# Optimization experiments

Hardware: AMD Instinct MI355X
Metric: run time of the kernel (lower is better)

## Reference

```python
import jax, jax.numpy as jnp
import numpy as np

B, S, DIN, DOUT = 4, 2048, 2048, 8192


def setup_inputs() -> dict:
    key = jax.random.key(0)
    kx, kw = jax.random.split(key)
    x = jax.random.normal(kx, (B, S, DIN), dtype=jnp.float32)
    # match torch init: uniform(-bound, bound), bound = sqrt(3) * 0.5 * in_features**-0.5
    bound = (3.0 ** 0.5) * 0.5 * DIN ** (-0.5)
    weight = jax.random.uniform(kw, (DOUT, DIN), dtype=jnp.float32, minval=-bound, maxval=bound)
    return {"x": x, "weight": weight}


def _rms_norm(x):
    # F.rms_norm with no weight: eps defaults to finfo(dtype).eps
    eps = jnp.finfo(x.dtype).eps
    return x * jax.lax.rsqrt(jnp.mean(x * x, axis=-1, keepdims=True) + eps)


def _act_quant(xn):
    # per-token int8 symmetric quant/dequant
    scale = 127.0 / jnp.maximum(jnp.max(jnp.abs(xn), axis=-1, keepdims=True), 1e-5)
    return jnp.clip(jnp.round(xn * scale), -128.0, 127.0) / scale


def _weight_quant(w):
    # ternary weight quant/dequant with global abs-mean scale
    scale = 1.0 / jnp.maximum(jnp.mean(jnp.abs(w)), 1e-5)
    return jnp.clip(jnp.round(w * scale), -1.0, 1.0) / scale


def reference(x, weight):
    xn = _rms_norm(x)
    # STE: forward uses quantized values, gradient flows through xn / weight
    x_q = xn + jax.lax.stop_gradient(_act_quant(xn) - xn)
    w_q = weight + jax.lax.stop_gradient(_weight_quant(weight) - weight)
    # F.linear: x @ w.T  -> [B, S, DOUT]
    return jnp.einsum('bsd,od->bso', x_q, w_q)
```

## Files before the change

kernel.cpp:

```cpp
#include <hip/hip_runtime.h>

typedef unsigned int u32;
typedef int i32x4 __attribute__((ext_vector_type(4)));

#define DIN 2048
#define DOUT 8192
#define MROWS 8192
#define NELEM_W (8192 * 2048)

#define WS_PART 0
#define WS_WFAC 16384
#define WS_ROWFAC 16640
#define WS_XQ 49408
#define WS_WQ (49408 + 16777216)

__global__ void k_wabs(const float* __restrict__ w, double* __restrict__ part) {
    const float4* w4 = (const float4*)w;
    const unsigned t = threadIdx.x, b = blockIdx.x;
    float s = 0.f;
    for (unsigned i = b * 256u + t; i < (NELEM_W / 4); i += 2048u * 256u) {
        float4 v = w4[i];
        s += fabsf(v.x) + fabsf(v.y) + fabsf(v.z) + fabsf(v.w);
    }
    double d = (double)s;
    #pragma unroll
    for (int o = 32; o; o >>= 1) d += __shfl_down(d, o);
    __shared__ double red[4];
    if ((t & 63u) == 0u) red[t >> 6] = d;
    __syncthreads();
    if (t == 0) part[b] = red[0] + red[1] + red[2] + red[3];
}

__global__ void k_wfin(const double* __restrict__ part, float* __restrict__ wfac) {
    const int t = threadIdx.x;
    double s = 0.0;
    #pragma unroll
    for (int j = 0; j < 8; ++j) s += part[t + j * 256];
    #pragma unroll
    for (int o = 32; o; o >>= 1) s += __shfl_down(s, o);
    __shared__ double red[4];
    if ((t & 63) == 0) red[t >> 6] = s;
    __syncthreads();
    if (t == 0) {
        double mean = (red[0] + red[1] + red[2] + red[3]) * (1.0 / (double)NELEM_W);
        *wfac = fmaxf((float)mean, 1e-5f);
    }
}

__global__ void k_prep(const float* __restrict__ w, const float* __restrict__ wfac,
                       u32* __restrict__ wq, const float* __restrict__ x,
                       u32* __restrict__ xq, float* __restrict__ rowfac) {
    const int t = threadIdx.x;
    if (blockIdx.x < 2048) {
        const float scale = 1.0f / *wfac;
        const float4* w4 = (const float4*)w;
        for (unsigned i = blockIdx.x * 256u + t; i < (NELEM_W / 4); i += 2048u * 256u) {
            float4 v = w4[i];
            int q0 = (int)fminf(fmaxf(rintf(v.x * scale), -1.f), 1.f);
            int q1 = (int)fminf(fmaxf(rintf(v.y * scale), -1.f), 1.f);
            int q2 = (int)fminf(fmaxf(rintf(v.z * scale), -1.f), 1.f);
            int q3 = (int)fminf(fmaxf(rintf(v.w * scale), -1.f), 1.f);
            wq[i] = (u32)(q0 & 255) | ((u32)(q1 & 255) << 8) |
                    ((u32)(q2 & 255) << 16) | ((u32)(q3 & 255) << 24);
        }
        return;
    }
    const int row = blockIdx.x - 2048;
    const float4* xr = (const float4*)(x + (size_t)row * DIN);
    float4 v0 = xr[t], v1 = xr[t + 256];
    float ss = v0.x * v0.x + v0.y * v0.y + v0.z * v0.z + v0.w * v0.w
             + v1.x * v1.x + v1.y * v1.y + v1.z * v1.z + v1.w * v1.w;
    __shared__ float red[4];
    #pragma unroll
    for (int o = 32; o; o >>= 1) ss += __shfl_down(ss, o);
    if ((t & 63) == 0) red[t >> 6] = ss;
    __syncthreads();
    ss = red[0] + red[1] + red[2] + red[3];
    const float r = 1.0f / sqrtf(ss * (1.0f / DIN) + 1.1920929e-7f);
    float xn[8] = {v0.x * r, v0.y * r, v0.z * r, v0.w * r,
                   v1.x * r, v1.y * r, v1.z * r, v1.w * r};
    float am = 0.f;
    #pragma unroll
    for (int j = 0; j < 8; ++j) am = fmaxf(am, fabsf(xn[j]));
    __syncthreads();
    #pragma unroll
    for (int o = 32; o; o >>= 1) am = fmaxf(am, __shfl_down(am, o));
    if ((t & 63) == 0) red[t >> 6] = am;
    __syncthreads();
    am = fmaxf(fmaxf(red[0], red[1]), fmaxf(red[2], red[3]));
    const float amc = fmaxf(am, 1e-5f);
    const float s = 127.0f / amc;
    int q[8];
    #pragma unroll
    for (int j = 0; j < 8; ++j)
        q[j] = (int)fminf(fmaxf(rintf(xn[j] * s), -128.f), 127.f);
    u32* xo = xq + (size_t)row * (DIN / 4);
    xo[t] = (u32)(q[0] & 255) | ((u32)(q[1] & 255) << 8) |
            ((u32)(q[2] & 255) << 16) | ((u32)(q[3] & 255) << 24);
    xo[t + 256] = (u32)(q[4] & 255) | ((u32)(q[5] & 255) << 8) |
                  ((u32)(q[6] & 255) << 16) | ((u32)(q[7] & 255) << 24);
    if (t == 0) rowfac[row] = amc * (1.0f / 127.0f);
}

__launch_bounds__(512, 2)
__global__ void k_gemm(const char* __restrict__ A, const char* __restrict__ Bw,
                       const float* __restrict__ rowfac, const float* __restrict__ wfac,
                       float* __restrict__ out) {
    __shared__ __attribute__((aligned(16))) char smb[131072];

    const int t = threadIdx.x;
    const int l = t & 63, w = t >> 6;
    const int wm = w >> 2, wn = w & 3;
    const int lr = l & 15, lc = l >> 4;
    const int laneRd = lr * 64 + ((lc ^ (lr & 3)) * 16);
    const int srow2 = t >> 2;
    const int sglog = ((t & 3) ^ (srow2 & 3)) * 16;

    const int bid = blockIdx.x;
    const int wg = (bid & 7) * 128 + (bid >> 3);
    const int bm = wg >> 5, bn = wg & 31;
    const char* Ab = A + (size_t)(bm * 256) * DIN;
    const char* Bb = Bw + (size_t)(bn * 256) * DIN;

    i32x4 acc[8][4] = {};
    i32x4 fa[4], fb[4];

#define STG1(gbase, opOff, tB, kh, s) do {                                        \
    _Pragma("unroll")                                                             \
    for (int j_ = 0; j_ < 2; ++j_)                                                \
        __builtin_amdgcn_global_load_lds(                                         \
            (const __attribute__((address_space(1))) void*)((gbase) + (size_t)(j_ * 128 + srow2) * DIN + (tB) + (kh) * 64 + sglog), \
            (__attribute__((address_space(3))) void*)(smb + (opOff) + (s) * 32768 + (kh) * 16384 + j_ * 8192 + t * 16), \
            16, 0, 0);                                                            \
} while (0)

#define NOGATE ((void)0)
#define VM6 asm volatile("s_waitcnt vmcnt(6)" ::: "memory")
#define VM0 asm volatile("s_waitcnt vmcnt(0)" ::: "memory")
#define NOSTG ((void)0)

#define PHASE(s, kh, mB, LOADB, STAGE_STMT, GATE_STMT) do {                       \
    const char* hbA_ = smb + (s) * 32768 + (kh) * 16384;                          \
    const char* hbB_ = hbA_ + 65536;                                              \
    _Pragma("unroll")                                                             \
    for (int i_ = 0; i_ < 4; ++i_)                                                \
        fa[i_] = *(const i32x4*)(hbA_ + (wm * 128 + ((mB) + i_) * 16) * 64 + laneRd); \
    if (LOADB) {                                                                  \
        _Pragma("unroll")                                                         \
        for (int n_ = 0; n_ < 4; ++n_)                                            \
            fb[n_] = *(const i32x4*)(hbB_ + (wn * 64 + n_ * 16) * 64 + laneRd);   \
    }                                                                             \
    STAGE_STMT;                                                                   \
    GATE_STMT;                                                                    \
    __builtin_amdgcn_s_barrier();                                                 \
    asm volatile("s_waitcnt lgkmcnt(0)" ::: "memory");                            \
    __builtin_amdgcn_s_setprio(1);                                                \
    _Pragma("unroll")                                                             \
    for (int m_ = 0; m_ < 4; ++m_)                                                \
        _Pragma("unroll")                                                         \
        for (int n_ = 0; n_ < 4; ++n_)                                            \
            acc[(mB) + m_][n_] = __builtin_amdgcn_mfma_i32_16x16x64_i8(           \
                fa[m_], fb[n_], acc[(mB) + m_][n_], 0, 0, 0);                     \
    __builtin_amdgcn_s_setprio(0);                                                \
    __builtin_amdgcn_s_barrier();                                                 \
} while (0)

    STG1(Ab, 0,     0,   0, 0);
    STG1(Bb, 65536, 0,   0, 0);
    STG1(Ab, 0,     0,   1, 0);
    STG1(Bb, 65536, 0,   1, 0);
    STG1(Bb, 65536, 128, 0, 1);
    STG1(Ab, 0,     128, 0, 1);
    STG1(Bb, 65536, 128, 1, 1);
    VM6;
    __builtin_amdgcn_s_barrier();

    #pragma unroll 1
    for (int it = 0; it < 7; ++it) {
        const int tB = it * 256;
        PHASE(0, 0, 0, true,  STG1(Ab, 0,     tB + 128, 1, 1), NOGATE);
        PHASE(0, 0, 4, false, STG1(Bb, 65536, tB + 256, 0, 0), NOGATE);
        PHASE(0, 1, 0, true,  STG1(Ab, 0,     tB + 256, 0, 0), NOGATE);
        PHASE(0, 1, 4, false, STG1(Bb, 65536, tB + 256, 1, 0), VM6);
        PHASE(1, 0, 0, true,  STG1(Ab, 0,     tB + 256, 1, 0), NOGATE);
        PHASE(1, 0, 4, false, STG1(Bb, 65536, tB + 384, 0, 1), NOGATE);
        PHASE(1, 1, 0, true,  STG1(Ab, 0,     tB + 384, 0, 1), NOGATE);
        PHASE(1, 1, 4, false, STG1(Bb, 65536, tB + 384, 1, 1), VM6);
    }
    PHASE(0, 0, 0, true,  STG1(Ab, 0, 1920, 1, 1), NOGATE);
    PHASE(0, 0, 4, false, NOSTG, NOGATE);
    PHASE(0, 1, 0, true,  NOSTG, NOGATE);
    PHASE(0, 1, 4, false, NOSTG, VM0);
    PHASE(1, 0, 0, true,  NOSTG, NOGATE);
    PHASE(1, 0, 4, false, NOSTG, NOGATE);
    PHASE(1, 1, 0, true,  NOSTG, NOGATE);
    PHASE(1, 1, 4, false, NOSTG, NOGATE);

    const float wf = *wfac;
    const int c0 = bn * 256 + wn * 64 + lr;
    #pragma unroll
    for (int m = 0; m < 8; ++m) {
        #pragma unroll
        for (int r = 0; r < 4; ++r) {
            const int grow = bm * 256 + wm * 128 + m * 16 + lc * 4 + r;
            const float s = rowfac[grow] * wf;
            const size_t ob = (size_t)grow * DOUT + c0;
            #pragma unroll
            for (int n = 0; n < 4; ++n)
                out[ob + n * 16] = (float)acc[m][n][r] * s;
        }
    }
#undef STG1
#undef PHASE
#undef NOGATE
#undef VM6
#undef VM0
#undef NOSTG
}

extern "C" void kernel_launch(void* const* d_in, const int* in_sizes, int n_in,
                              void* d_out, int out_size, void* d_ws, size_t ws_size,
                              hipStream_t stream) {
    const float* x = (const float*)d_in[0];
    const float* wt = (const float*)d_in[1];
    float* out = (float*)d_out;
    char* ws = (char*)d_ws;

    double* part = (double*)(ws + WS_PART);
    float* wfac = (float*)(ws + WS_WFAC);
    float* rowfac = (float*)(ws + WS_ROWFAC);
    u32* xq = (u32*)(ws + WS_XQ);
    u32* wq = (u32*)(ws + WS_WQ);

    k_wabs<<<2048, 256, 0, stream>>>(wt, part);
    k_wfin<<<1, 256, 0, stream>>>(part, wfac);
    k_prep<<<2048 + MROWS, 256, 0, stream>>>(wt, wfac, wq, x, xq, rowfac);
    k_gemm<<<1024, 512, 0, stream>>>((const char*)xq, (const char*)wq, rowfac, wfac, out);
}
```

Measured before the change: 216.7 us.

## Shrink GEMM tile to 128x128 with 32x32x32 int8 MFMA and 4 waves

Replaces the 256x256 block tile with 8 waves by a 128x128 tile with 4 waves, each computing a 64x64 sub-tile using 32x32x32 int8 MFMAs instead of 16x16x64. LDS use halves to 64KB, which could allow more blocks per CU, and the grid grows to 4096 blocks with a new swizzled block mapping and a reworked vmcnt-gated double-buffer schedule. The aim is better occupancy and wave balance. The cost is lower arithmetic intensity per block, meaning more global/L2 traffic for the A and B operands, plus a different epilogue store pattern.

```diff
diff --git a/kernel.cpp b/kernel.cpp
--- a/kernel.cpp
+++ b/kernel.cpp
@@ -2,6 +2,7 @@
 
 typedef unsigned int u32;
 typedef int i32x4 __attribute__((ext_vector_type(4)));
+typedef int i32x16 __attribute__((ext_vector_type(16)));
 
 #define DIN 2048
 #define DOUT 8192
@@ -102,120 +103,125 @@
     if (t == 0) rowfac[row] = amc * (1.0f / 127.0f);
 }
 
-__launch_bounds__(512, 2)
+__launch_bounds__(256, 2)
 __global__ void k_gemm(const char* __restrict__ A, const char* __restrict__ Bw,
                        const float* __restrict__ rowfac, const float* __restrict__ wfac,
                        float* __restrict__ out) {
-    __shared__ __attribute__((aligned(16))) char smb[131072];
+    __shared__ __attribute__((aligned(16))) char smb[65536];
 
     const int t = threadIdx.x;
     const int l = t & 63, w = t >> 6;
-    const int wm = w >> 2, wn = w & 3;
-    const int lr = l & 15, lc = l >> 4;
-    const int laneRd = lr * 64 + ((lc ^ (lr & 3)) * 16);
-    const int srow2 = t >> 2;
-    const int sglog = ((t & 3) ^ (srow2 & 3)) * 16;
+    const int wm = w >> 1, wn = w & 1;
+    const int la = l & 31, lhi = l >> 5;
+    const int o0 = ((lhi ^ ((la >> 1) & 3)) * 16);
+    const int o1 = o0 ^ 32;
+    const int aR0 = (wm * 64 + la) * 64, aR1 = (wm * 64 + 32 + la) * 64;
+    const int bR0 = (wn * 64 + la) * 64, bR1 = (wn * 64 + 32 + la) * 64;
+    const int sgl = ((t & 3) ^ ((t >> 3) & 3)) * 16;
+    const int srw = t >> 2;
 
     const int bid = blockIdx.x;
-    const int wg = (bid & 7) * 128 + (bid >> 3);
-    const int bm = wg >> 5, bn = wg & 31;
-    const char* Ab = A + (size_t)(bm * 256) * DIN;
-    const char* Bb = Bw + (size_t)(bn * 256) * DIN;
-
-    i32x4 acc[8][4] = {};
-    i32x4 fa[4], fb[4];
-
-#define STG1(gbase, opOff, tB, kh, s) do {                                        \
+    const int wg = (bid & 7) * 512 + (bid >> 3);
+    const int bm = wg >> 6, bn = wg & 63;
+    const char* Ab = A + (size_t)(bm * 128) * DIN;
+    const char* Bb = Bw + (size_t)(bn * 128) * DIN;
+
+    i32x16 acc[2][2] = {};
+
+#define STGK(tB, kh, s) do {                                                      \
     _Pragma("unroll")                                                             \
     for (int j_ = 0; j_ < 2; ++j_)                                                \
         __builtin_amdgcn_global_load_lds(                                         \
-            (const __attribute__((address_space(1))) void*)((gbase) + (size_t)(j_ * 128 + srow2) * DIN + (tB) + (kh) * 64 + sglog), \
-            (__attribute__((address_space(3))) void*)(smb + (opOff) + (s) * 32768 + (kh) * 16384 + j_ * 8192 + t * 16), \
+            (const __attribute__((address_space(1))) void*)(Ab + (size_t)(j_ * 64 + srw) * DIN + (tB) + (kh) * 64 + sgl), \
+            (__attribute__((address_space(3))) void*)(smb + (s) * 16384 + (kh) * 8192 + j_ * 4096 + t * 16), \
+            16, 0, 0);                                                            \
+    _Pragma("unroll")                                                             \
+    for (int j_ = 0; j_ < 2; ++j_)                                                \
+        __builtin_amdgcn_global_load_lds(                                         \
+            (const __attribute__((address_space(1))) void*)(Bb + (size_t)(j_ * 64 + srw) * DIN + (tB) + (kh) * 64 + sgl), \
+            (__attribute__((address_space(3))) void*)(smb + 32768 + (s) * 16384 + (kh) * 8192 + j_ * 4096 + t * 16), \
             16, 0, 0);                                                            \
 } while (0)
 
 #define NOGATE ((void)0)
-#define VM6 asm volatile("s_waitcnt vmcnt(6)" ::: "memory")
-#define VM0 asm volatile("s_waitcnt vmcnt(0)" ::: "memory")
 #define NOSTG ((void)0)
-
-#define PHASE(s, kh, mB, LOADB, STAGE_STMT, GATE_STMT) do {                       \
-    const char* hbA_ = smb + (s) * 32768 + (kh) * 16384;                          \
-    const char* hbB_ = hbA_ + 65536;                                              \
-    _Pragma("unroll")                                                             \
-    for (int i_ = 0; i_ < 4; ++i_)                                                \
-        fa[i_] = *(const i32x4*)(hbA_ + (wm * 128 + ((mB) + i_) * 16) * 64 + laneRd); \
-    if (LOADB) {                                                                  \
-        _Pragma("unroll")                                                         \
-        for (int n_ = 0; n_ < 4; ++n_)                                            \
-            fb[n_] = *(const i32x4*)(hbB_ + (wn * 64 + n_ * 16) * 64 + laneRd);   \
-    }                                                                             \
+#define VM(n) asm volatile("s_waitcnt vmcnt(" #n ")" ::: "memory")
+
+#define PHASE(s, kh, STAGE_STMT, GATE_STMT) do {                                  \
+    const char* aB_ = smb + (s) * 16384 + (kh) * 8192;                            \
+    const char* bB_ = aB_ + 32768;                                                \
+    i32x4 fa0_[2], fa1_[2], fb0_[2], fb1_[2];                                     \
+    fa0_[0] = *(const i32x4*)(aB_ + aR0 + o0);                                    \
+    fa0_[1] = *(const i32x4*)(aB_ + aR1 + o0);                                    \
+    fb0_[0] = *(const i32x4*)(bB_ + bR0 + o0);                                    \
+    fb0_[1] = *(const i32x4*)(bB_ + bR1 + o0);                                    \
+    fa1_[0] = *(const i32x4*)(aB_ + aR0 + o1);                                    \
+    fa1_[1] = *(const i32x4*)(aB_ + aR1 + o1);                                    \
+    fb1_[0] = *(const i32x4*)(bB_ + bR0 + o1);                                    \
+    fb1_[1] = *(const i32x4*)(bB_ + bR1 + o1);                                    \
     STAGE_STMT;                                                                   \
     GATE_STMT;                                                                    \
     __builtin_amdgcn_s_barrier();                                                 \
     asm volatile("s_waitcnt lgkmcnt(0)" ::: "memory");                            \
     __builtin_amdgcn_s_setprio(1);                                                \
     _Pragma("unroll")                                                             \
-    for (int m_ = 0; m_ < 4; ++m_)                                                \
+    for (int mt_ = 0; mt_ < 2; ++mt_)                                             \
         _Pragma("unroll")                                                         \
-        for (int n_ = 0; n_ < 4; ++n_)                                            \
-            acc[(mB) + m_][n_] = __builtin_amdgcn_mfma_i32_16x16x64_i8(           \
-                fa[m_], fb[n_], acc[(mB) + m_][n_], 0, 0, 0);                     \
+        for (int nt_ = 0; nt_ < 2; ++nt_)                                         \
+            acc[mt_][nt_] = __builtin_amdgcn_mfma_i32_32x32x32_i8(                \
+                fa0_[mt_], fb0_[nt_], acc[mt_][nt_], 0, 0, 0);                    \
+    _Pragma("unroll")                                                             \
+    for (int mt_ = 0; mt_ < 2; ++mt_)                                             \
+        _Pragma("unroll")                                                         \
+        for (int nt_ = 0; nt_ < 2; ++nt_)                                         \
+            acc[mt_][nt_] = __builtin_amdgcn_mfma_i32_32x32x32_i8(                \
+                fa1_[mt_], fb1_[nt_], acc[mt_][nt_], 0, 0, 0);                    \
     __builtin_amdgcn_s_setprio(0);                                                \
     __builtin_amdgcn_s_barrier();                                                 \
 } while (0)
 
-    STG1(Ab, 0,     0,   0, 0);
-    STG1(Bb, 65536, 0,   0, 0);
-    STG1(Ab, 0,     0,   1, 0);
-    STG1(Bb, 65536, 0,   1, 0);
-    STG1(Bb, 65536, 128, 0, 1);
-    STG1(Ab, 0,     128, 0, 1);
-    STG1(Bb, 65536, 128, 1, 1);
-    VM6;
+    STGK(0, 0, 0);
+    STGK(0, 1, 0);
+    STGK(128, 0, 1);
+    VM(4);
     __builtin_amdgcn_s_barrier();
 
     #pragma unroll 1
-    for (int it = 0; it < 7; ++it) {
-        const int tB = it * 256;
-        PHASE(0, 0, 0, true,  STG1(Ab, 0,     tB + 128, 1, 1), NOGATE);
-        PHASE(0, 0, 4, false, STG1(Bb, 65536, tB + 256, 0, 0), NOGATE);
-        PHASE(0, 1, 0, true,  STG1(Ab, 0,     tB + 256, 0, 0), NOGATE);
-        PHASE(0, 1, 4, false, STG1(Bb, 65536, tB + 256, 1, 0), VM6);
-        PHASE(1, 0, 0, true,  STG1(Ab, 0,     tB + 256, 1, 0), NOGATE);
-        PHASE(1, 0, 4, false, STG1(Bb, 65536, tB + 384, 0, 1), NOGATE);
-        PHASE(1, 1, 0, true,  STG1(Ab, 0,     tB + 384, 0, 1), NOGATE);
-        PHASE(1, 1, 4, false, STG1(Bb, 65536, tB + 384, 1, 1), VM6);
-    }
-    PHASE(0, 0, 0, true,  STG1(Ab, 0, 1920, 1, 1), NOGATE);
-    PHASE(0, 0, 4, false, NOSTG, NOGATE);
-    PHASE(0, 1, 0, true,  NOSTG, NOGATE);
-    PHASE(0, 1, 4, false, NOSTG, VM0);
-    PHASE(1, 0, 0, true,  NOSTG, NOGATE);
-    PHASE(1, 0, 4, false, NOSTG, NOGATE);
-    PHASE(1, 1, 0, true,  NOSTG, NOGATE);
-    PHASE(1, 1, 4, false, NOSTG, NOGATE);
+    for (int it = 0; it < 14; ++it) {
+        const int s = it & 1;
+        const int tB = it * 128;
+        if (s == 0) {
+            PHASE(0, 0, STGK(tB + 128, 1, 1), VM(8));
+            PHASE(0, 1, STGK(tB + 256, 0, 0), VM(8));
+        } else {
+            PHASE(1, 0, STGK(tB + 128, 1, 0), VM(8));
+            PHASE(1, 1, STGK(tB + 256, 0, 1), VM(8));
+        }
+    }
+    PHASE(0, 0, STGK(1920, 1, 1), VM(8));
+    PHASE(0, 1, NOSTG, VM(4));
+    PHASE(1, 0, NOSTG, VM(0));
+    PHASE(1, 1, NOSTG, NOGATE);
 
     const float wf = *wfac;
-    const int c0 = bn * 256 + wn * 64 + lr;
-    #pragma unroll
-    for (int m = 0; m < 8; ++m) {
+    const int gcol0 = bn * 128 + wn * 64 + la;
+    #pragma unroll
+    for (int mt = 0; mt < 2; ++mt) {
         #pragma unroll
-        for (int r = 0; r < 4; ++r) {
-            const int grow = bm * 256 + wm * 128 + m * 16 + lc * 4 + r;
+        for (int reg = 0; reg < 16; ++reg) {
+            const int grow = bm * 128 + wm * 64 + mt * 32 +
+                             (reg & 3) + 8 * (reg >> 2) + 4 * lhi;
             const float s = rowfac[grow] * wf;
-            const size_t ob = (size_t)grow * DOUT + c0;
-            #pragma unroll
-            for (int n = 0; n < 4; ++n)
-                out[ob + n * 16] = (float)acc[m][n][r] * s;
+            const size_t ob = (size_t)grow * DOUT + gcol0;
+            out[ob]      = (float)acc[mt][0][reg] * s;
+            out[ob + 32] = (float)acc[mt][1][reg] * s;
         }
     }
-#undef STG1
+#undef STGK
 #undef PHASE
 #undef NOGATE
-#undef VM6
-#undef VM0
 #undef NOSTG
+#undef VM
 }
 
 extern "C" void kernel_launch(void* const* d_in, const int* in_sizes, int n_in,
@@ -235,5 +241,5 @@
     k_wabs<<<2048, 256, 0, stream>>>(wt, part);
     k_wfin<<<1, 256, 0, stream>>>(part, wfac);
     k_prep<<<2048 + MROWS, 256, 0, stream>>>(wt, wfac, wq, x, xq, rowfac);
-    k_gemm<<<1024, 512, 0, stream>>>((const char*)xq, (const char*)wq, rowfac, wfac, out);
-}
+    k_gemm<<<4096, 256, 0, stream>>>((const char*)xq, (const char*)wq, rowfac, wfac, out);
+}
```

Result: slower. 265.8 us (+22.7%).
